# Optimization experiments

Hardware: AMD Instinct MI355X
Metric: run time of the kernel (lower is better)

The kernel has to match this reference:

```python
import jax, jax.numpy as jnp
import numpy as np

B, IN, H = 8192, 1024, 2048

def setup_inputs() -> dict:
    key = jax.random.key(0)
    k1, k2, k3, k4, k5 = jax.random.split(key, 5)
    prev_state = jax.random.normal(k1, (B, H), dtype=jnp.float32)
    x = jax.random.normal(k2, (B, IN), dtype=jnp.float32)
    input_weights = jax.random.normal(k3, (H, IN), dtype=jnp.float32) / IN ** 0.5
    input_bias = jnp.zeros((H,), dtype=jnp.float32)
    recurrent_weights = jax.random.normal(k4, (H, H), dtype=jnp.float32) / H ** 0.5
    U_z = jax.random.normal(k5, (H, H), dtype=jnp.float32) / H ** 0.5
    b_u = jnp.zeros((H,), dtype=jnp.float32)
    return {"prev_state": prev_state, "input": x,
            "input_weights": input_weights, "input_bias": input_bias,
            "recurrent_weights": recurrent_weights, "U_z": U_z, "b_u": b_u}

def reference(prev_state, input, input_weights, input_bias, recurrent_weights, U_z, b_u):
    # z = tanh(x @ W_x^T + b_x)
    z = jnp.tanh(input @ input_weights.T + input_bias)
    # u = sigmoid(h @ W_h^T + z @ U_z^T + b_u)
    u = jax.nn.sigmoid(prev_state @ recurrent_weights.T + z @ U_z.T + b_u)
    # convex combination of previous state and candidate
    state = u * prev_state + (1.0 - u) * z
    return state
```

## Files before the change

### kernel.cpp

```cpp
#include <hip/hip_runtime.h>
#include <hip/hip_bf16.h>
#include <cstdint>
#include <cstddef>

#define DEVFN static __device__ __forceinline__

typedef __attribute__((ext_vector_type(8))) short bf16x8;
typedef __attribute__((ext_vector_type(4))) float f32x4;

static constexpr int kB = 8192;
static constexpr int kIN = 1024;
static constexpr int kH = 2048;

DEVFN unsigned short f32_to_bf16(float f) {
  union { float f; unsigned int u; } v; v.f = f;
  unsigned int x = v.u;
  x += 0x7fffu + ((x >> 16) & 1u);
  return (unsigned short)(x >> 16);
}
DEVFN float bf16_to_f32(unsigned short u) {
  union { unsigned int u; float f; } v; v.u = (unsigned int)u << 16;
  return v.f;
}

__global__ void cast_all(const float* __restrict__ x, const float* __restrict__ Wx,
                         const float* __restrict__ Wh, const float* __restrict__ Uz,
                         const float* __restrict__ h,
                         unsigned short* __restrict__ xb, unsigned short* __restrict__ Wxb,
                         unsigned short* __restrict__ Wcat, unsigned short* __restrict__ Acat) {
  const long i = (long)blockIdx.x * blockDim.x + threadIdx.x;
  const float* src; unsigned short* dst; int sh, stride, off; long li;
  if (i < 2097152L)      { li = i;            src = x;  dst = xb;   sh = 8; stride = 1024; off = 0; }
  else if (i < 2621440L) { li = i - 2097152L; src = Wx; dst = Wxb;  sh = 8; stride = 1024; off = 0; }
  else if (i < 3670016L) { li = i - 2621440L; src = Wh; dst = Wcat; sh = 9; stride = 4096; off = 0; }
  else if (i < 4718592L) { li = i - 3670016L; src = Uz; dst = Wcat; sh = 9; stride = 4096; off = 2048; }
  else                   { li = i - 4718592L; src = h;  dst = Acat; sh = 9; stride = 4096; off = 0; }
  float4 v = *(const float4*)(src + li * 4);
  const long row = li >> sh;
  const long col = (li & ((1L << sh) - 1)) * 4;
  unsigned short* d = dst + row * stride + off + col;
  ushort4 o;
  o.x = f32_to_bf16(v.x); o.y = f32_to_bf16(v.y);
  o.z = f32_to_bf16(v.z); o.w = f32_to_bf16(v.w);
  *(ushort4*)d = o;
}

typedef const __attribute__((address_space(1))) unsigned int* gptr_t;
typedef __attribute__((address_space(3))) unsigned int* lptr_t;
DEVFN void gload16(const unsigned short* g, unsigned short* l) {
  __builtin_amdgcn_global_load_lds((gptr_t)g, (lptr_t)l, 16, 0, 0);
}

DEVFN void bar() { __builtin_amdgcn_s_barrier(); }
#define LGKM0() asm volatile("s_waitcnt lgkmcnt(0)" ::: "memory")
#define VMC4()  asm volatile("s_waitcnt vmcnt(4)" ::: "memory")


template<int BUF, int QM>
DEVFN void ldA(bf16x8 (&a)[4][2], const unsigned short* lds, int wm, int lr, int lg) {
  const unsigned short* rg = lds + (size_t)(BUF * 4 + wm) * 8192;
#pragma unroll
  for (int mi = 0; mi < 4; ++mi) {
    const int rl = QM * 64 + mi * 16 + lr;
#pragma unroll
    for (int kk = 0; kk < 2; ++kk) {
      const int kel = (kk * 32 + lg * 8) ^ ((rl & 7) * 8);
      a[mi][kk] = *(const bf16x8*)(rg + rl * 64 + kel);
    }
  }
}

template<int BUF, int QN>
DEVFN void ldB(bf16x8 (&b)[4][2], const unsigned short* lds, int wn, int lr, int lg) {
  const unsigned short* rg = lds + (size_t)(BUF * 4 + 2 + (wn >> 1)) * 8192;
#pragma unroll
  for (int ni = 0; ni < 2; ++ni) {
    const int n = QN * 2 + ni;
    const int cl = (wn & 1) * 64 + n * 16 + lr;
#pragma unroll
    for (int kk = 0; kk < 2; ++kk) {
      const int kel = (kk * 32 + lg * 8) ^ ((cl & 7) * 8);
      b[n][kk] = *(const bf16x8*)(rg + cl * 64 + kel);
    }
  }
}

template<int QM, int QN>
DEVFN void mfmaQ(f32x4 (&acc)[8][4], bf16x8 (&a)[4][2], bf16x8 (&b)[4][2]) {
  __builtin_amdgcn_s_setprio(1);
#pragma unroll
  for (int mi = 0; mi < 4; ++mi)
#pragma unroll
    for (int ni = 0; ni < 2; ++ni)
#pragma unroll
      for (int kk = 0; kk < 2; ++kk)
        acc[QM * 4 + mi][QN * 2 + ni] = __builtin_amdgcn_mfma_f32_16x16x32_bf16(
            a[mi][kk], b[QN * 2 + ni][kk], acc[QM * 4 + mi][QN * 2 + ni], 0, 0, 0);
  __builtin_amdgcn_s_setprio(0);
}

template<int EPI>
__global__ __launch_bounds__(512, 1)
void gemm256(const unsigned short* __restrict__ A,
             const unsigned short* __restrict__ W,
             const float* __restrict__ bias,
             int M, int K,
             unsigned short* __restrict__ zOut,
             const unsigned short* __restrict__ hzBuf, int ldhz,
             float* __restrict__ out, int ldo)
{
  __shared__ unsigned short lds[8][8192];
  unsigned short* L = &lds[0][0];

  const int nTM = M >> 8;
  const int bm = blockIdx.x % nTM, bn = blockIdx.x / nTM;
  const int rowBase = bm << 8, colBase = bn << 8;

  const int t = threadIdx.x;
  const int l = t & 63;
  const int w = t >> 6;
  const int lr = l & 15, lg = l >> 4;
  const int wm = w >> 2, wn = w & 3;

  const int srow = t >> 3;
  const int scol = (t & 7) * 8;
  const int kcSrc = scol ^ ((srow & 7) * 8);
  const unsigned short* gA = A + (size_t)(rowBase + srow) * K + kcSrc;
  const unsigned short* gB = W + (size_t)(colBase + srow) * K + kcSrc;

#define STAGE(BUF, OP, HALF, KT) do {                                          \
    const unsigned short* gs = ((OP) ? gB : gA)                                \
        + (size_t)((HALF) * 128) * K + (size_t)(KT) * 64;                      \
    unsigned short* ld = L + (size_t)((BUF) * 4 + (OP) * 2 + (HALF)) * 8192    \
        + w * 512;                                                             \
    gload16(gs, ld);                                                           \
    gload16(gs + (size_t)64 * K, ld + 4096);                                   \
  } while (0)

  f32x4 acc[8][4] = {};
  bf16x8 a[4][2], b[4][2];

  STAGE(0, 0, 0, 0); STAGE(0, 0, 1, 0); STAGE(0, 1, 0, 0); STAGE(0, 1, 1, 0);
  STAGE(1, 1, 0, 1); STAGE(1, 1, 1, 1);
  VMC4();
  bar();

  const int NP = K >> 7;
  for (int i = 0; i < NP; ++i) {
    const bool more = (i + 1 < NP);
    const int ktb1  = 2 * i + 1;
    const int kt0n  = more ? 2 * i + 2 : 2 * i;
    const int kt1n  = more ? 2 * i + 3 : 2 * i + 1;

    ldA<0, 0>(a, L, wm, lr, lg); ldB<0, 0>(b, L, wn, lr, lg);
    STAGE(1, 0, 0, ktb1);
    bar(); LGKM0();
    mfmaQ<0, 0>(acc, a, b);
    bar();
    ldB<0, 1>(b, L, wn, lr, lg);
    STAGE(1, 0, 1, ktb1);
    bar(); LGKM0();
    mfmaQ<0, 1>(acc, a, b);
    bar();
    ldA<0, 1>(a, L, wm, lr, lg);
    STAGE(0, 1, 0, kt0n);
    bar(); LGKM0();
    mfmaQ<1, 0>(acc, a, b);
    bar();
    STAGE(0, 1, 1, kt0n);
    bar(); LGKM0();
    mfmaQ<1, 1>(acc, a, b);
    VMC4();
    bar();
    ldA<1, 0>(a, L, wm, lr, lg); ldB<1, 0>(b, L, wn, lr, lg);
    STAGE(0, 0, 0, kt0n);
    bar(); LGKM0();
    mfmaQ<0, 0>(acc, a, b);
    bar();
    ldB<1, 1>(b, L, wn, lr, lg);
    STAGE(0, 0, 1, kt0n);
    bar(); LGKM0();
    mfmaQ<0, 1>(acc, a, b);
    bar();
    ldA<1, 1>(a, L, wm, lr, lg);
    STAGE(1, 1, 0, kt1n);
    bar(); LGKM0();
    mfmaQ<1, 0>(acc, a, b);
    bar();
    STAGE(1, 1, 1, kt1n);
    bar(); LGKM0();
    mfmaQ<1, 1>(acc, a, b);
    VMC4();
    bar();
  }
#undef STAGE

#pragma unroll
  for (int m = 0; m < 8; ++m) {
    const int r0 = rowBase + wm * 128 + m * 16 + lg * 4;
#pragma unroll
    for (int n = 0; n < 4; ++n) {
      const int c = colBase + wn * 64 + n * 16 + lr;
      const float bs = bias[c];
#pragma unroll
      for (int q = 0; q < 4; ++q) {
        const int r = r0 + q;
        const float pre = acc[m][n][q] + bs;
        if (EPI == 0) {
          zOut[(size_t)r * ldhz + c] = f32_to_bf16(tanhf(pre));
        } else {
          const float u = 1.0f / (1.0f + __expf(-pre));
          const float hv = bf16_to_f32(hzBuf[(size_t)r * ldhz + c]);
          const float zv = bf16_to_f32(hzBuf[(size_t)r * ldhz + 2048 + c]);
          out[(size_t)r * ldo + c] = u * hv + (1.0f - u) * zv;
        }
      }
    }
  }
}

extern "C" void kernel_launch(void* const* d_in, const int* in_sizes, int n_in,
                              void* d_out, int out_size, void* d_ws, size_t ws_size,
                              hipStream_t stream) {
  const float* h  = (const float*)d_in[0];
  const float* x  = (const float*)d_in[1];
  const float* Wx = (const float*)d_in[2];
  const float* bx = (const float*)d_in[3];
  const float* Wh = (const float*)d_in[4];
  const float* Uz = (const float*)d_in[5];
  const float* bu = (const float*)d_in[6];
  float* out = (float*)d_out;

  unsigned short* ws   = (unsigned short*)d_ws;
  unsigned short* xb   = ws;
  unsigned short* Wxb  = xb + (size_t)kB * kIN;
  unsigned short* Wcat = Wxb + (size_t)kH * kIN;
  unsigned short* Acat = Wcat + (size_t)kH * 2 * kH;

  cast_all<<<34816, 256, 0, stream>>>(x, Wx, Wh, Uz, h, xb, Wxb, Wcat, Acat);

  const int grid = (kB / 256) * (kH / 256);

  gemm256<0><<<grid, 512, 0, stream>>>(
      xb, Wxb, bx, kB, kIN, Acat + kH, nullptr, 2 * kH, nullptr, 0);

  gemm256<1><<<grid, 512, 0, stream>>>(
      Acat, Wcat, bu, kB, 2 * kH, nullptr, Acat, 2 * kH, out, kH);
}
```

Before: 211.4 us.

## Restructure GEMM prefetch to stage full A/B tiles in grouped batches

```diff
diff --git a/kernel.cpp b/kernel.cpp
--- a/kernel.cpp
+++ b/kernel.cpp
@@ -53,7 +53,8 @@
 
 DEVFN void bar() { __builtin_amdgcn_s_barrier(); }
 #define LGKM0() asm volatile("s_waitcnt lgkmcnt(0)" ::: "memory")
-#define VMC4()  asm volatile("s_waitcnt vmcnt(4)" ::: "memory")
+#define LGKM8() asm volatile("s_waitcnt lgkmcnt(8)" ::: "memory")
+#define VMC8()  asm volatile("s_waitcnt vmcnt(8)" ::: "memory")
 
 
 template<int BUF, int QM>
@@ -128,72 +129,69 @@
   const unsigned short* gA = A + (size_t)(rowBase + srow) * K + kcSrc;
   const unsigned short* gB = W + (size_t)(colBase + srow) * K + kcSrc;
 
-#define STAGE(BUF, OP, HALF, KT) do {                                          \
-    const unsigned short* gs = ((OP) ? gB : gA)                                \
-        + (size_t)((HALF) * 128) * K + (size_t)(KT) * 64;                      \
-    unsigned short* ld = L + (size_t)((BUF) * 4 + (OP) * 2 + (HALF)) * 8192    \
-        + w * 512;                                                             \
+#define STAGE2(BUF, OP, KT) do {                                               \
+    const unsigned short* gs = ((OP) ? gB : gA) + (size_t)(KT) * 64;           \
+    unsigned short* ld = L + (size_t)((BUF) * 4 + (OP) * 2) * 8192 + w * 512;  \
     gload16(gs, ld);                                                           \
     gload16(gs + (size_t)64 * K, ld + 4096);                                   \
+    gload16(gs + (size_t)128 * K, ld + 8192);                                  \
+    gload16(gs + (size_t)192 * K, ld + 8192 + 4096);                           \
   } while (0)
 
   f32x4 acc[8][4] = {};
   bf16x8 a[4][2], b[4][2];
 
-  STAGE(0, 0, 0, 0); STAGE(0, 0, 1, 0); STAGE(0, 1, 0, 0); STAGE(0, 1, 1, 0);
-  STAGE(1, 1, 0, 1); STAGE(1, 1, 1, 1);
-  VMC4();
+  STAGE2(0, 0, 0); STAGE2(0, 1, 0);
+  STAGE2(1, 1, 1); STAGE2(1, 0, 1);
+  VMC8();
   bar();
 
   const int NP = K >> 7;
   for (int i = 0; i < NP; ++i) {
     const bool more = (i + 1 < NP);
-    const int ktb1  = 2 * i + 1;
-    const int kt0n  = more ? 2 * i + 2 : 2 * i;
-    const int kt1n  = more ? 2 * i + 3 : 2 * i + 1;
+    const int kt0n = more ? 2 * i + 2 : 2 * i;
+    const int kt1n = more ? 2 * i + 3 : 2 * i + 1;
 
     ldA<0, 0>(a, L, wm, lr, lg); ldB<0, 0>(b, L, wn, lr, lg);
-    STAGE(1, 0, 0, ktb1);
+    LGKM8();
     bar(); LGKM0();
     mfmaQ<0, 0>(acc, a, b);
     bar();
     ldB<0, 1>(b, L, wn, lr, lg);
-    STAGE(1, 0, 1, ktb1);
     bar(); LGKM0();
     mfmaQ<0, 1>(acc, a, b);
     bar();
     ldA<0, 1>(a, L, wm, lr, lg);
-    STAGE(0, 1, 0, kt0n);
+    STAGE2(0, 1, kt0n);
     bar(); LGKM0();
     mfmaQ<1, 0>(acc, a, b);
     bar();
-    STAGE(0, 1, 1, kt0n);
+    STAGE2(0, 0, kt0n);
     bar(); LGKM0();
     mfmaQ<1, 1>(acc, a, b);
-    VMC4();
+    VMC8();
     bar();
     ldA<1, 0>(a, L, wm, lr, lg); ldB<1, 0>(b, L, wn, lr, lg);
-    STAGE(0, 0, 0, kt0n);
+    LGKM8();
     bar(); LGKM0();
     mfmaQ<0, 0>(acc, a, b);
     bar();
     ldB<1, 1>(b, L, wn, lr, lg);
-    STAGE(0, 0, 1, kt0n);
     bar(); LGKM0();
     mfmaQ<0, 1>(acc, a, b);
     bar();
     ldA<1, 1>(a, L, wm, lr, lg);
-    STAGE(1, 1, 0, kt1n);
+    STAGE2(1, 1, kt1n);
     bar(); LGKM0();
     mfmaQ<1, 0>(acc, a, b);
     bar();
-    STAGE(1, 1, 1, kt1n);
+    STAGE2(1, 0, kt1n);
     bar(); LGKM0();
     mfmaQ<1, 1>(acc, a, b);
-    VMC4();
-    bar();
-  }
-#undef STAGE
+    VMC8();
+    bar();
+  }
+#undef STAGE2
 
 #pragma unroll
   for (int m = 0; m < 8; ++m) {
```

Result: no change. 215.5 us (+1.9%).

## Switch GEMM to 32x32x16 MFMA tiles and swizzle block order

Applied to the files above, without the earlier changes.

```diff
diff --git a/kernel.cpp b/kernel.cpp
--- a/kernel.cpp
+++ b/kernel.cpp
@@ -6,7 +6,7 @@
 #define DEVFN static __device__ __forceinline__
 
 typedef __attribute__((ext_vector_type(8))) short bf16x8;
-typedef __attribute__((ext_vector_type(4))) float f32x4;
+typedef __attribute__((ext_vector_type(16))) float f32x16;
 
 static constexpr int kB = 8192;
 static constexpr int kIN = 1024;
@@ -57,45 +57,39 @@
 
 
 template<int BUF, int QM>
-DEVFN void ldA(bf16x8 (&a)[4][2], const unsigned short* lds, int wm, int lr, int lg) {
+DEVFN void ldA(bf16x8 (&a)[2][4], const unsigned short* lds, int wm, int l) {
   const unsigned short* rg = lds + (size_t)(BUF * 4 + wm) * 8192;
 #pragma unroll
-  for (int mi = 0; mi < 4; ++mi) {
-    const int rl = QM * 64 + mi * 16 + lr;
-#pragma unroll
-    for (int kk = 0; kk < 2; ++kk) {
-      const int kel = (kk * 32 + lg * 8) ^ ((rl & 7) * 8);
-      a[mi][kk] = *(const bf16x8*)(rg + rl * 64 + kel);
+  for (int mi = 0; mi < 2; ++mi) {
+    const int rl = QM * 64 + mi * 32 + (l & 31);
+#pragma unroll
+    for (int ks = 0; ks < 4; ++ks) {
+      const int kel = (ks * 16 + (l >> 5) * 8) ^ ((rl & 7) * 8);
+      a[mi][ks] = *(const bf16x8*)(rg + rl * 64 + kel);
     }
   }
 }
 
 template<int BUF, int QN>
-DEVFN void ldB(bf16x8 (&b)[4][2], const unsigned short* lds, int wn, int lr, int lg) {
+DEVFN void ldB(bf16x8 (&b)[2][4], const unsigned short* lds, int wn, int l) {
   const unsigned short* rg = lds + (size_t)(BUF * 4 + 2 + (wn >> 1)) * 8192;
-#pragma unroll
-  for (int ni = 0; ni < 2; ++ni) {
-    const int n = QN * 2 + ni;
-    const int cl = (wn & 1) * 64 + n * 16 + lr;
-#pragma unroll
-    for (int kk = 0; kk < 2; ++kk) {
-      const int kel = (kk * 32 + lg * 8) ^ ((cl & 7) * 8);
-      b[n][kk] = *(const bf16x8*)(rg + cl * 64 + kel);
-    }
+  const int cl = (wn & 1) * 64 + QN * 32 + (l & 31);
+#pragma unroll
+  for (int ks = 0; ks < 4; ++ks) {
+    const int kel = (ks * 16 + (l >> 5) * 8) ^ ((cl & 7) * 8);
+    b[QN][ks] = *(const bf16x8*)(rg + cl * 64 + kel);
   }
 }
 
 template<int QM, int QN>
-DEVFN void mfmaQ(f32x4 (&acc)[8][4], bf16x8 (&a)[4][2], bf16x8 (&b)[4][2]) {
+DEVFN void mfmaQ(f32x16 (&acc)[4][2], bf16x8 (&a)[2][4], bf16x8 (&b)[2][4]) {
   __builtin_amdgcn_s_setprio(1);
 #pragma unroll
-  for (int mi = 0; mi < 4; ++mi)
-#pragma unroll
-    for (int ni = 0; ni < 2; ++ni)
-#pragma unroll
-      for (int kk = 0; kk < 2; ++kk)
-        acc[QM * 4 + mi][QN * 2 + ni] = __builtin_amdgcn_mfma_f32_16x16x32_bf16(
-            a[mi][kk], b[QN * 2 + ni][kk], acc[QM * 4 + mi][QN * 2 + ni], 0, 0, 0);
+  for (int ks = 0; ks < 4; ++ks)
+#pragma unroll
+    for (int mi = 0; mi < 2; ++mi)
+      acc[QM * 2 + mi][QN] = __builtin_amdgcn_mfma_f32_32x32x16_bf16(
+          a[mi][ks], b[QN][ks], acc[QM * 2 + mi][QN], 0, 0, 0);
   __builtin_amdgcn_s_setprio(0);
 }
 
@@ -113,13 +107,14 @@
   unsigned short* L = &lds[0][0];
 
   const int nTM = M >> 8;
-  const int bm = blockIdx.x % nTM, bn = blockIdx.x / nTM;
+  const int bid = blockIdx.x;
+  const int swz = (bid & 7) * (gridDim.x >> 3) + (bid >> 3);
+  const int bm = swz % nTM, bn = swz / nTM;
   const int rowBase = bm << 8, colBase = bn << 8;
 
   const int t = threadIdx.x;
   const int l = t & 63;
   const int w = t >> 6;
-  const int lr = l & 15, lg = l >> 4;
   const int wm = w >> 2, wn = w & 3;
 
   const int srow = t >> 3;
@@ -137,8 +132,8 @@
     gload16(gs + (size_t)64 * K, ld + 4096);                                   \
   } while (0)
 
-  f32x4 acc[8][4] = {};
-  bf16x8 a[4][2], b[4][2];
+  f32x16 acc[4][2] = {};
+  bf16x8 a[2][4], b[2][4];
 
   STAGE(0, 0, 0, 0); STAGE(0, 0, 1, 0); STAGE(0, 1, 0, 0); STAGE(0, 1, 1, 0);
   STAGE(1, 1, 0, 1); STAGE(1, 1, 1, 1);
@@ -148,21 +143,21 @@
   const int NP = K >> 7;
   for (int i = 0; i < NP; ++i) {
     const bool more = (i + 1 < NP);
-    const int ktb1  = 2 * i + 1;
-    const int kt0n  = more ? 2 * i + 2 : 2 * i;
-    const int kt1n  = more ? 2 * i + 3 : 2 * i + 1;
-
-    ldA<0, 0>(a, L, wm, lr, lg); ldB<0, 0>(b, L, wn, lr, lg);
+    const int ktb1 = 2 * i + 1;
+    const int kt0n = more ? 2 * i + 2 : 2 * i;
+    const int kt1n = more ? 2 * i + 3 : 2 * i + 1;
+
+    ldA<0, 0>(a, L, wm, l); ldB<0, 0>(b, L, wn, l);
     STAGE(1, 0, 0, ktb1);
     bar(); LGKM0();
     mfmaQ<0, 0>(acc, a, b);
     bar();
-    ldB<0, 1>(b, L, wn, lr, lg);
+    ldB<0, 1>(b, L, wn, l);
     STAGE(1, 0, 1, ktb1);
     bar(); LGKM0();
     mfmaQ<0, 1>(acc, a, b);
     bar();
-    ldA<0, 1>(a, L, wm, lr, lg);
+    ldA<0, 1>(a, L, wm, l);
     STAGE(0, 1, 0, kt0n);
     bar(); LGKM0();
     mfmaQ<1, 0>(acc, a, b);
@@ -172,17 +167,17 @@
     mfmaQ<1, 1>(acc, a, b);
     VMC4();
     bar();
-    ldA<1, 0>(a, L, wm, lr, lg); ldB<1, 0>(b, L, wn, lr, lg);
+    ldA<1, 0>(a, L, wm, l); ldB<1, 0>(b, L, wn, l);
     STAGE(0, 0, 0, kt0n);
     bar(); LGKM0();
     mfmaQ<0, 0>(acc, a, b);
     bar();
-    ldB<1, 1>(b, L, wn, lr, lg);
+    ldB<1, 1>(b, L, wn, l);
     STAGE(0, 0, 1, kt0n);
     bar(); LGKM0();
     mfmaQ<0, 1>(acc, a, b);
     bar();
-    ldA<1, 1>(a, L, wm, lr, lg);
+    ldA<1, 1>(a, L, wm, l);
     STAGE(1, 1, 0, kt1n);
     bar(); LGKM0();
     mfmaQ<1, 0>(acc, a, b);
@@ -196,16 +191,16 @@
 #undef STAGE
 
 #pragma unroll
-  for (int m = 0; m < 8; ++m) {
-    const int r0 = rowBase + wm * 128 + m * 16 + lg * 4;
-#pragma unroll
-    for (int n = 0; n < 4; ++n) {
-      const int c = colBase + wn * 64 + n * 16 + lr;
-      const float bs = bias[c];
-#pragma unroll
-      for (int q = 0; q < 4; ++q) {
-        const int r = r0 + q;
-        const float pre = acc[m][n][q] + bs;
+  for (int nt = 0; nt < 2; ++nt) {
+    const int c = colBase + wn * 64 + nt * 32 + (l & 31);
+    const float bs = bias[c];
+#pragma unroll
+    for (int mt = 0; mt < 4; ++mt) {
+      const int rb = rowBase + wm * 128 + mt * 32 + 4 * (l >> 5);
+#pragma unroll
+      for (int reg = 0; reg < 16; ++reg) {
+        const int r = rb + (reg & 3) + 8 * (reg >> 2);
+        const float pre = acc[mt][nt][reg] + bs;
         if (EPI == 0) {
           zOut[(size_t)r * ldhz + c] = f32_to_bf16(tanhf(pre));
         } else {
```

Result: slower. 326.4 us (+54.4%).
